# Kernel tuning notes

Measured on AMD Instinct MI355X. Metric: run time of the kernel, lower is better.

## Reference

```python
import jax, jax.numpy as jnp
import numpy as np
import math

B, C, H, W = 8, 64, 256, 256
E, NH = 256, 8
HD = E // NH  # 32


def get_coords(h, w):
    xx, yy = jnp.meshgrid(jnp.arange(h, dtype=jnp.float32), jnp.arange(w, dtype=jnp.float32), indexing='ij')
    return jnp.stack((xx.reshape(-1), yy.reshape(-1)), axis=-1)  # [N, 2]


def setup_inputs() -> dict:
    key = jax.random.key(0)
    ks = jax.random.split(key, 12)
    def xavier(k, shape):
        fan_out, fan_in = shape
        a = math.sqrt(6.0 / (fan_in + fan_out))
        return jax.random.uniform(k, shape, jnp.float32, -a, a)
    x = jax.random.normal(ks[0], (B, C, H, W), jnp.float32)
    z = jax.random.normal(ks[1], (B, C), jnp.float32)
    pos = jax.random.uniform(ks[2], (B, NH, 2), jnp.float32) * (H - 1)
    Wq = xavier(ks[3], (E, C)); bq = jnp.zeros((E,), jnp.float32)
    Wk = xavier(ks[4], (E, C)); bk = jnp.zeros((E,), jnp.float32)
    Wv = xavier(ks[5], (E, C)); bv = jnp.zeros((E,), jnp.float32)
    Wp = xavier(ks[6], (HD, 2)); bp = jax.random.uniform(ks[7], (HD,), jnp.float32, -1.0, 1.0) / math.sqrt(2.0)
    return {"x": x, "z": z, "pos": pos, "Wq": Wq, "bq": bq, "Wk": Wk, "bk": bk,
            "Wv": Wv, "bv": bv, "Wp": Wp, "bp": bp}


def reference(x, z, pos, Wq, bq, Wk, bk, Wv, bv, Wp, bp):
    b, c, h, w = x.shape
    n = h * w
    x_flat = x.reshape(b, c, n).transpose(0, 2, 1)          # [B, N, C]
    pos_grid = get_coords(h, w)                              # [N, 2]
    q = (z @ Wq.T + bq).reshape(b, NH, HD)                   # [B, H, hd]
    k = (x_flat @ Wk.T + bk).reshape(b, n, NH, HD)           # [B, N, H, hd]
    # relative-position modulation of keys
    rel = pos_grid[None, :, None, :] - pos[:, None, :, :]    # [B, N, H, 2]
    qxk = rel @ Wp.T + bp                                    # [B, N, H, hd]
    k = k * qxk
    v = x_flat @ Wv.T + bv                                   # [B, N, E]
    attn_logits = jnp.einsum('bhc,bnhc->bnh', q, k) / math.sqrt(HD)
    attention = jax.nn.softmax(attn_logits, axis=1)          # softmax over N
    pos_out = jnp.einsum('bnh,nx->bhx', attention, pos_grid) # [B, H, 2]
    values = jnp.einsum('bnh,bnc->bhc', attention, v)        # [B, H, E]
    return (values, pos_out)
```

## Files before the change

kernel.cpp:

```cpp
#include <hip/hip_runtime.h>

#define NN    65536
#define NSUB  256
#define NBLK  (NN/NSUB)
#define WPAD  260

#define OFF_W   0
#define SZ_W    (8*64*24)
#define OFF_CJ  (OFF_W + SZ_W)
#define SZ_CJ   (8*24)
#define OFF_PM  (OFF_CJ + SZ_CJ)
#define SZ_P    (8*NBLK*8)
#define OFF_PL  (OFF_PM + SZ_P)
#define OFF_PSP (OFF_PL + SZ_P)
#define OFF_PSX (OFF_PSP + 2*SZ_P)

#define SMEM1_FLOATS (64*WPAD + 8*256 + 1536 + 64)
#define SMEM1_BYTES  (SMEM1_FLOATS*4)

__global__ __launch_bounds__(64) void prep_kernel(
    const float* __restrict__ z,  const float* __restrict__ Wq, const float* __restrict__ bq,
    const float* __restrict__ Wk, const float* __restrict__ bk,
    const float* __restrict__ Wp, const float* __restrict__ bp,
    float* __restrict__ Weff, float* __restrict__ Cj)
{
  const int h = blockIdx.x, b = blockIdx.y, t = threadIdx.x;
  __shared__ float q[32];
  if (t < 32) {
    const int e = h*32 + t;
    float a = bq[e];
    const float* zr = z + b*64;
    const float* wr = Wq + e*64;
    #pragma unroll 8
    for (int c = 0; c < 64; ++c) a += zr[c]*wr[c];
    q[t] = a;
  }
  __syncthreads();
  {
    const int c = t;
    float w0 = 0.f, w1 = 0.f, w2 = 0.f;
    #pragma unroll 4
    for (int hd = 0; hd < 32; ++hd) {
      const float qk = q[hd] * Wk[(h*32+hd)*64 + c];
      w0 += qk * bp[hd];
      w1 += qk * Wp[hd*2+0];
      w2 += qk * Wp[hd*2+1];
    }
    float* o = Weff + (b*64 + c)*24 + h*3;
    o[0] = w0; o[1] = w1; o[2] = w2;
  }
  if (t < 3) {
    float s = 0.f;
    for (int hd = 0; hd < 32; ++hd) {
      const float m = (t == 0) ? bp[hd] : Wp[hd*2 + (t-1)];
      s += q[hd] * m * bk[h*32+hd];
    }
    Cj[b*24 + h*3 + t] = s;
  }
}

__global__ __launch_bounds__(256) void main_kernel(
    const float* __restrict__ x, const float* __restrict__ pos,
    const float* __restrict__ Weff, const float* __restrict__ Cj,
    float* __restrict__ Pm, float* __restrict__ Pl,
    float* __restrict__ Psp, float* __restrict__ Psx)
{
  extern __shared__ float sm[];
  float* xs  = sm;
  float* ps  = xs + 64*WPAD;
  float* wsw = ps + 8*256;
  float* red = wsw + 1536;
  const int t   = threadIdx.x;
  const int blk = blockIdx.x;
  const int b   = blockIdx.y;
  const int n0  = blk * NSUB;
  const int wid = t >> 6, lid = t & 63;

  {
    const float* xb = x + (size_t)b*64*NN + n0;
    #pragma unroll
    for (int r = 0; r < 16; ++r) {
      const int f  = t + r*256;
      const int c  = f >> 6;
      const int p4 = (f & 63) << 2;
      const float4 v = *(const float4*)(xb + (size_t)c*NN + p4);
      *(float4*)(xs + c*WPAD + p4) = v;
    }
    const float* wsrc = Weff + b*1536;
    #pragma unroll
    for (int r = 0; r < 6; ++r) wsw[t + r*256] = wsrc[t + r*256];
  }

  float cj[24];
  #pragma unroll
  for (int k = 0; k < 24; ++k) cj[k] = Cj[b*24 + k];
  float rxh[8], py[8];
  #pragma unroll
  for (int h = 0; h < 8; ++h) {
    rxh[h] = (float)blk - pos[(b*8+h)*2 + 0];
    py[h]  = pos[(b*8+h)*2 + 1];
  }

  __syncthreads();

  float2 acc2[12];
  #pragma unroll
  for (int j = 0; j < 12; ++j) acc2[j] = make_float2(cj[2*j], cj[2*j+1]);
  #pragma unroll 2
  for (int c = 0; c < 64; ++c) {
    const float xv = xs[c*WPAD + t];
    const float2* wr = (const float2*)(wsw + c*24);
    #pragma unroll
    for (int j = 0; j < 12; ++j) {
      acc2[j].x += wr[j].x * xv;
      acc2[j].y += wr[j].y * xv;
    }
  }
  const float* acc = (const float*)acc2;
  const float tyf = (float)t;
  float lg[8];
  #pragma unroll
  for (int h = 0; h < 8; ++h)
    lg[h] = (acc[h*3+0] + rxh[h]*acc[h*3+1] + (tyf - py[h])*acc[h*3+2]) * 0.17677669529663687f;

  float mh[8];
  #pragma unroll
  for (int h = 0; h < 8; ++h) {
    float m = lg[h];
    #pragma unroll
    for (int off = 32; off >= 1; off >>= 1) m = fmaxf(m, __shfl_xor(m, off, 64));
    mh[h] = m;
  }
  if (lid == 0) {
    #pragma unroll
    for (int h = 0; h < 8; ++h) red[h*4 + wid] = mh[h];
  }
  __syncthreads();

  #pragma unroll
  for (int h = 0; h < 8; ++h) {
    const float M = fmaxf(fmaxf(red[h*4+0], red[h*4+1]), fmaxf(red[h*4+2], red[h*4+3]));
    mh[h] = M;
    ps[h*256 + t] = __expf(lg[h] - M);
  }
  __syncthreads();

  {
    const int h0 = wid*2;
    const float4 pa = *(const float4*)(ps + h0*256 + 4*lid);
    const float4 pb = *(const float4*)(ps + (h0+1)*256 + 4*lid);
    const float j0 = (float)(4*lid);
    float s0a = pa.x + pa.y + pa.z + pa.w;
    float s1a = pa.x*j0 + pa.y*(j0+1.f) + pa.z*(j0+2.f) + pa.w*(j0+3.f);
    float s0b = pb.x + pb.y + pb.z + pb.w;
    float s1b = pb.x*j0 + pb.y*(j0+1.f) + pb.z*(j0+2.f) + pb.w*(j0+3.f);
    #pragma unroll
    for (int off = 32; off >= 1; off >>= 1) {
      s0a += __shfl_xor(s0a, off, 64);
      s1a += __shfl_xor(s1a, off, 64);
      s0b += __shfl_xor(s0b, off, 64);
      s1b += __shfl_xor(s1b, off, 64);
    }
    if (lid == 0) {
      const int base = (b*NBLK + blk)*8;
      const float blkf = (float)blk;
      Pm[base+h0]   = mh[h0];   Pl[base+h0]   = s0a;
      Psp[(base+h0)*2+0]   = blkf*s0a;  Psp[(base+h0)*2+1]   = s1a;
      Pm[base+h0+1] = mh[h0+1]; Pl[base+h0+1] = s0b;
      Psp[(base+h0+1)*2+0] = blkf*s0b;  Psp[(base+h0+1)*2+1] = s1b;
    }
  }

  float aB[8];
  #pragma unroll
  for (int h = 0; h < 8; ++h) aB[h] = 0.f;
  {
    const int nq = wid*64;
    const float* xr = xs + lid*WPAD + nq;
    #pragma unroll 2
    for (int j = 0; j < 16; ++j) {
      const float4 xv = *(const float4*)(xr + 4*j);
      #pragma unroll
      for (int h = 0; h < 8; ++h) {
        const float4 pv = *(const float4*)(ps + h*256 + nq + 4*j);
        aB[h] += pv.x*xv.x + pv.y*xv.y + pv.z*xv.z + pv.w*xv.w;
      }
    }
  }
  __syncthreads();
  {
    float* part = sm;
    #pragma unroll
    for (int h = 0; h < 8; ++h) part[(wid*8 + h)*64 + lid] = aB[h];
  }
  __syncthreads();
  {
    const int pb = (b*NBLK + blk)*8;
    #pragma unroll
    for (int r = 0; r < 2; ++r) {
      const int idx = t + 256*r;
      const float s = sm[idx] + sm[512+idx] + sm[1024+idx] + sm[1536+idx];
      Psx[(size_t)pb*64 + idx] = s;
    }
  }
}

__global__ __launch_bounds__(1024) void finish_kernel(
    const float* __restrict__ Pm, const float* __restrict__ Pl,
    const float* __restrict__ Psp, const float* __restrict__ Psx,
    const float* __restrict__ Wv, const float* __restrict__ bv,
    float* __restrict__ out)
{
  const int h = blockIdx.x, b = blockIdx.y, t = threadIdx.x;
  __shared__ float al[256];
  __shared__ float redm[32];
  __shared__ float sxl[1024];
  __shared__ float SXs[64];
  const int wid = t >> 6, lid = t & 63;

  float m_t = 0.f;
  if (t < 256) {
    m_t = Pm[(b*NBLK + t)*8 + h];
    float mm = m_t;
    #pragma unroll
    for (int off = 32; off >= 1; off >>= 1) mm = fmaxf(mm, __shfl_xor(mm, off, 64));
    if (lid == 0) redm[wid] = mm;
  }
  __syncthreads();
  const float M = fmaxf(fmaxf(redm[0], redm[1]), fmaxf(redm[2], redm[3]));
  if (t < 256) {
    const int pbase = (b*NBLK + t)*8 + h;
    const float a = __expf(m_t - M);
    al[t] = a;
    float lt  = Pl[pbase] * a;
    float sxt = Psp[pbase*2+0] * a;
    float syt = Psp[pbase*2+1] * a;
    #pragma unroll
    for (int off = 32; off >= 1; off >>= 1) {
      lt  += __shfl_xor(lt,  off, 64);
      sxt += __shfl_xor(sxt, off, 64);
      syt += __shfl_xor(syt, off, 64);
    }
    if (lid == 0) { redm[4+wid] = lt; redm[8+wid] = sxt; redm[12+wid] = syt; }
  }
  __syncthreads();
  const float L = redm[4]+redm[5]+redm[6]+redm[7];
  const float invL = 1.0f / L;

  {
    const int c = lid, g = wid;
    float acc = 0.f;
    #pragma unroll
    for (int k = 0; k < 16; ++k) {
      const int blk = g*16 + k;
      acc += Psx[((size_t)(b*NBLK + blk)*8 + h)*64 + c] * al[blk];
    }
    sxl[g*64 + c] = acc;
  }
  __syncthreads();
  if (t < 64) {
    float s = 0.f;
    #pragma unroll
    for (int g = 0; g < 16; ++g) s += sxl[g*64 + t];
    SXs[t] = s * invL;
  }
  __syncthreads();

  if (t < 256) {
    float v = bv[t];
    const float* wvr = Wv + t*64;
    #pragma unroll 8
    for (int c2 = 0; c2 < 64; ++c2) v += wvr[c2] * SXs[c2];
    out[(b*8+h)*256 + t] = v;
  }
  if (t == 0) {
    const float SPx = redm[8]+redm[9]+redm[10]+redm[11];
    const float SPy = redm[12]+redm[13]+redm[14]+redm[15];
    out[16384 + (b*8+h)*2 + 0] = SPx * invL;
    out[16384 + (b*8+h)*2 + 1] = SPy * invL;
  }
}

extern "C" void kernel_launch(void* const* d_in, const int* in_sizes, int n_in,
                              void* d_out, int out_size, void* d_ws, size_t ws_size,
                              hipStream_t stream)
{
  const float* x   = (const float*)d_in[0];
  const float* z   = (const float*)d_in[1];
  const float* pos = (const float*)d_in[2];
  const float* Wq  = (const float*)d_in[3];
  const float* bq  = (const float*)d_in[4];
  const float* Wk  = (const float*)d_in[5];
  const float* bk  = (const float*)d_in[6];
  const float* Wv  = (const float*)d_in[7];
  const float* bv  = (const float*)d_in[8];
  const float* Wp  = (const float*)d_in[9];
  const float* bp  = (const float*)d_in[10];
  float* out = (float*)d_out;
  float* ws  = (float*)d_ws;

  float* Weff = ws + OFF_W;
  float* Cj   = ws + OFF_CJ;
  float* Pm   = ws + OFF_PM;
  float* Pl   = ws + OFF_PL;
  float* Psp  = ws + OFF_PSP;
  float* Psx  = ws + OFF_PSX;

  (void)hipFuncSetAttribute((const void*)main_kernel,
                            hipFuncAttributeMaxDynamicSharedMemorySize, SMEM1_BYTES);

  prep_kernel  <<<dim3(8,8),    64,   0,           stream>>>(z, Wq, bq, Wk, bk, Wp, bp, Weff, Cj);
  main_kernel  <<<dim3(NBLK,8), 256,  SMEM1_BYTES, stream>>>(x, pos, Weff, Cj, Pm, Pl, Psp, Psx);
  finish_kernel<<<dim3(8,8),    1024, 0,           stream>>>(Pm, Pl, Psp, Psx, Wv, bv, out);
}
```

Baseline: 264.7 us.

## Load x into registers, use wave readlane for P·x, split final reduction

The main kernel now has each thread load its own 64 channel values straight into registers and compute the logits from those, reading the weight rows directly from global memory. x is stored transposed in shared memory with odd padding. The P·x product broadcasts softmax weights across the wave with readlane instead of staging them in shared memory, and the per-block sums are built from wave shuffles. The single 64-block finish kernel becomes a two-stage reduction across 512 blocks and then 64 blocks, to spread the merge of partials over more of the GPU. The trade-offs are higher register pressure from the 64-float array, uncached-style weight reads from global, and one extra kernel launch.

```diff
diff --git a/kernel.cpp b/kernel.cpp
--- a/kernel.cpp
+++ b/kernel.cpp
@@ -3,7 +3,7 @@
 #define NN    65536
 #define NSUB  256
 #define NBLK  (NN/NSUB)
-#define WPAD  260
+#define CPAD  65
 
 #define OFF_W   0
 #define SZ_W    (8*64*24)
@@ -14,8 +14,11 @@
 #define OFF_PL  (OFF_PM + SZ_P)
 #define OFF_PSP (OFF_PL + SZ_P)
 #define OFF_PSX (OFF_PSP + 2*SZ_P)
-
-#define SMEM1_FLOATS (64*WPAD + 8*256 + 1536 + 64)
+#define SZ_PSX  (8*NBLK*8*64)
+#define OFF_Q   (OFF_PSX + SZ_PSX)
+#define QSTR    68
+
+#define SMEM1_FLOATS (NSUB*CPAD + 128)
 #define SMEM1_BYTES  (SMEM1_FLOATS*4)
 
 __global__ __launch_bounds__(64) void prep_kernel(
@@ -59,7 +62,7 @@
   }
 }
 
-__global__ __launch_bounds__(256) void main_kernel(
+__global__ __launch_bounds__(256, 2) void main_kernel(
     const float* __restrict__ x, const float* __restrict__ pos,
     const float* __restrict__ Weff, const float* __restrict__ Cj,
     float* __restrict__ Pm, float* __restrict__ Pl,
@@ -67,132 +70,115 @@
 {
   extern __shared__ float sm[];
   float* xs  = sm;
-  float* ps  = xs + 64*WPAD;
-  float* wsw = ps + 8*256;
-  float* red = wsw + 1536;
+  float* red = sm + NSUB*CPAD;
   const int t   = threadIdx.x;
   const int blk = blockIdx.x;
   const int b   = blockIdx.y;
   const int n0  = blk * NSUB;
   const int wid = t >> 6, lid = t & 63;
 
-  {
-    const float* xb = x + (size_t)b*64*NN + n0;
-    #pragma unroll
-    for (int r = 0; r < 16; ++r) {
-      const int f  = t + r*256;
-      const int c  = f >> 6;
-      const int p4 = (f & 63) << 2;
-      const float4 v = *(const float4*)(xb + (size_t)c*NN + p4);
-      *(float4*)(xs + c*WPAD + p4) = v;
-    }
-    const float* wsrc = Weff + b*1536;
-    #pragma unroll
-    for (int r = 0; r < 6; ++r) wsw[t + r*256] = wsrc[t + r*256];
-  }
-
-  float cj[24];
-  #pragma unroll
-  for (int k = 0; k < 24; ++k) cj[k] = Cj[b*24 + k];
-  float rxh[8], py[8];
-  #pragma unroll
-  for (int h = 0; h < 8; ++h) {
-    rxh[h] = (float)blk - pos[(b*8+h)*2 + 0];
-    py[h]  = pos[(b*8+h)*2 + 1];
-  }
-
-  __syncthreads();
-
-  float2 acc2[12];
-  #pragma unroll
-  for (int j = 0; j < 12; ++j) acc2[j] = make_float2(cj[2*j], cj[2*j+1]);
-  #pragma unroll 2
-  for (int c = 0; c < 64; ++c) {
-    const float xv = xs[c*WPAD + t];
-    const float2* wr = (const float2*)(wsw + c*24);
-    #pragma unroll
-    for (int j = 0; j < 12; ++j) {
-      acc2[j].x += wr[j].x * xv;
-      acc2[j].y += wr[j].y * xv;
-    }
-  }
-  const float* acc = (const float*)acc2;
-  const float tyf = (float)t;
+  float vx[64];
+  {
+    const float* xg = x + (size_t)b*64*NN + n0 + t;
+    #pragma unroll
+    for (int c = 0; c < 64; ++c) vx[c] = xg[(size_t)c*NN];
+    #pragma unroll
+    for (int c = 0; c < 64; ++c) xs[t*CPAD + c] = vx[c];
+  }
+
+  float acc[24];
+  {
+    const float* cjp = Cj + b*24;
+    #pragma unroll
+    for (int k = 0; k < 24; ++k) acc[k] = cjp[k];
+  }
+  {
+    const float* wb = Weff + b*1536;
+    #pragma unroll
+    for (int c = 0; c < 64; ++c) {
+      const float xv = vx[c];
+      const float* wr = wb + c*24;
+      #pragma unroll
+      for (int k = 0; k < 24; ++k) acc[k] += wr[k]*xv;
+    }
+  }
   float lg[8];
-  #pragma unroll
-  for (int h = 0; h < 8; ++h)
-    lg[h] = (acc[h*3+0] + rxh[h]*acc[h*3+1] + (tyf - py[h])*acc[h*3+2]) * 0.17677669529663687f;
-
-  float mh[8];
+  {
+    const float gx = (float)blk;
+    const float ty = (float)t;
+    #pragma unroll
+    for (int h = 0; h < 8; ++h) {
+      const float rx = gx - pos[(b*8+h)*2 + 0];
+      const float ry = ty - pos[(b*8+h)*2 + 1];
+      lg[h] = (acc[h*3+0] + rx*acc[h*3+1] + ry*acc[h*3+2]) * 0.17677669529663687f;
+    }
+  }
+
   #pragma unroll
   for (int h = 0; h < 8; ++h) {
     float m = lg[h];
     #pragma unroll
     for (int off = 32; off >= 1; off >>= 1) m = fmaxf(m, __shfl_xor(m, off, 64));
-    mh[h] = m;
-  }
-  if (lid == 0) {
-    #pragma unroll
-    for (int h = 0; h < 8; ++h) red[h*4 + wid] = mh[h];
-  }
-  __syncthreads();
-
+    if (lid == 0) red[h*4 + wid] = m;
+  }
+  __syncthreads();
+
+  float p[8];
   #pragma unroll
   for (int h = 0; h < 8; ++h) {
     const float M = fmaxf(fmaxf(red[h*4+0], red[h*4+1]), fmaxf(red[h*4+2], red[h*4+3]));
-    mh[h] = M;
-    ps[h*256 + t] = __expf(lg[h] - M);
-  }
-  __syncthreads();
-
-  {
-    const int h0 = wid*2;
-    const float4 pa = *(const float4*)(ps + h0*256 + 4*lid);
-    const float4 pb = *(const float4*)(ps + (h0+1)*256 + 4*lid);
-    const float j0 = (float)(4*lid);
-    float s0a = pa.x + pa.y + pa.z + pa.w;
-    float s1a = pa.x*j0 + pa.y*(j0+1.f) + pa.z*(j0+2.f) + pa.w*(j0+3.f);
-    float s0b = pb.x + pb.y + pb.z + pb.w;
-    float s1b = pb.x*j0 + pb.y*(j0+1.f) + pb.z*(j0+2.f) + pb.w*(j0+3.f);
-    #pragma unroll
-    for (int off = 32; off >= 1; off >>= 1) {
-      s0a += __shfl_xor(s0a, off, 64);
-      s1a += __shfl_xor(s1a, off, 64);
-      s0b += __shfl_xor(s0b, off, 64);
-      s1b += __shfl_xor(s1b, off, 64);
-    }
-    if (lid == 0) {
-      const int base = (b*NBLK + blk)*8;
-      const float blkf = (float)blk;
-      Pm[base+h0]   = mh[h0];   Pl[base+h0]   = s0a;
-      Psp[(base+h0)*2+0]   = blkf*s0a;  Psp[(base+h0)*2+1]   = s1a;
-      Pm[base+h0+1] = mh[h0+1]; Pl[base+h0+1] = s0b;
-      Psp[(base+h0+1)*2+0] = blkf*s0b;  Psp[(base+h0+1)*2+1] = s1b;
-    }
+    p[h] = __expf(lg[h] - M);
+  }
+  {
+    const float lf = (float)lid;
+    #pragma unroll
+    for (int h = 0; h < 8; ++h) {
+      float sp  = p[h];
+      float spj = p[h]*lf;
+      #pragma unroll
+      for (int off = 32; off >= 1; off >>= 1) {
+        sp  += __shfl_xor(sp,  off, 64);
+        spj += __shfl_xor(spj, off, 64);
+      }
+      if (lid == 0) { red[32 + h*4 + wid] = sp; red[64 + h*4 + wid] = spj; }
+    }
+  }
+  __syncthreads();
+
+  if (t < 8) {
+    const int base = (b*NBLK + blk)*8 + t;
+    const float M = fmaxf(fmaxf(red[t*4+0], red[t*4+1]), fmaxf(red[t*4+2], red[t*4+3]));
+    float L = 0.f, SJ = 0.f;
+    #pragma unroll
+    for (int w = 0; w < 4; ++w) {
+      const float sp = red[32 + t*4 + w];
+      L  += sp;
+      SJ += 64.0f*(float)w*sp + red[64 + t*4 + w];
+    }
+    Pm[base] = M;
+    Pl[base] = L;
+    Psp[base*2+0] = (float)blk * L;
+    Psp[base*2+1] = SJ;
   }
 
   float aB[8];
   #pragma unroll
   for (int h = 0; h < 8; ++h) aB[h] = 0.f;
   {
-    const int nq = wid*64;
-    const float* xr = xs + lid*WPAD + nq;
-    #pragma unroll 2
-    for (int j = 0; j < 16; ++j) {
-      const float4 xv = *(const float4*)(xr + 4*j);
+    const float* xcol = xs + wid*64*CPAD + lid;
+    #pragma unroll 8
+    for (int j = 0; j < 64; ++j) {
+      const float xv = xcol[j*CPAD];
       #pragma unroll
       for (int h = 0; h < 8; ++h) {
-        const float4 pv = *(const float4*)(ps + h*256 + nq + 4*j);
-        aB[h] += pv.x*xv.x + pv.y*xv.y + pv.z*xv.z + pv.w*xv.w;
+        const float pj = __int_as_float(__builtin_amdgcn_readlane(__float_as_int(p[h]), j));
+        aB[h] = fmaf(pj, xv, aB[h]);
       }
     }
   }
   __syncthreads();
-  {
-    float* part = sm;
-    #pragma unroll
-    for (int h = 0; h < 8; ++h) part[(wid*8 + h)*64 + lid] = aB[h];
-  }
+  #pragma unroll
+  for (int h = 0; h < 8; ++h) sm[(wid*8 + h)*64 + lid] = aB[h];
   __syncthreads();
   {
     const int pb = (b*NBLK + blk)*8;
@@ -205,79 +191,108 @@
   }
 }
 
-__global__ __launch_bounds__(1024) void finish_kernel(
+__global__ __launch_bounds__(256) void reduce1_kernel(
     const float* __restrict__ Pm, const float* __restrict__ Pl,
     const float* __restrict__ Psp, const float* __restrict__ Psx,
-    const float* __restrict__ Wv, const float* __restrict__ bv,
+    float* __restrict__ Q)
+{
+  const int g = blockIdx.x, h = blockIdx.y, b = blockIdx.z, t = threadIdx.x;
+  __shared__ float al[32];
+  __shared__ float mgs;
+  __shared__ float sums[3];
+  __shared__ float sxl[256];
+  const int base = (b*NBLK + g*32)*8 + h;
+
+  float m_t = -1e30f;
+  if (t < 32) m_t = Pm[base + t*8];
+  if (t < 64) {
+    float mm = m_t;
+    #pragma unroll
+    for (int off = 16; off >= 1; off >>= 1) mm = fmaxf(mm, __shfl_xor(mm, off, 64));
+    if (t == 0) mgs = mm;
+  }
+  __syncthreads();
+  const float Mg = mgs;
+  if (t < 32) {
+    const float a = __expf(m_t - Mg);
+    al[t] = a;
+    float lt  = Pl[base + t*8] * a;
+    float sx  = Psp[(base + t*8)*2 + 0] * a;
+    float sy  = Psp[(base + t*8)*2 + 1] * a;
+    #pragma unroll
+    for (int off = 16; off >= 1; off >>= 1) {
+      lt += __shfl_xor(lt, off, 64);
+      sx += __shfl_xor(sx, off, 64);
+      sy += __shfl_xor(sy, off, 64);
+    }
+    if (t == 0) { sums[0] = lt; sums[1] = sx; sums[2] = sy; }
+  }
+  __syncthreads();
+  {
+    const int c = t & 63, g2 = t >> 6;
+    float acc = 0.f;
+    #pragma unroll
+    for (int i = 0; i < 8; ++i) {
+      const int k = g2*8 + i;
+      acc += al[k] * Psx[(size_t)(base + k*8)*64 + c];
+    }
+    sxl[g2*64 + c] = acc;
+  }
+  __syncthreads();
+  float* q = Q + ((b*8 + h)*8 + g)*QSTR;
+  if (t < 64) q[4+t] = sxl[t] + sxl[64+t] + sxl[128+t] + sxl[192+t];
+  if (t == 0) { q[0] = Mg; q[1] = sums[0]; q[2] = sums[1]; q[3] = sums[2]; }
+}
+
+__global__ __launch_bounds__(64) void reduce2_kernel(
+    const float* __restrict__ Q, const float* __restrict__ Wv, const float* __restrict__ bv,
     float* __restrict__ out)
 {
   const int h = blockIdx.x, b = blockIdx.y, t = threadIdx.x;
-  __shared__ float al[256];
-  __shared__ float redm[32];
-  __shared__ float sxl[1024];
+  __shared__ float qm[8], bl[8], l8[8], sx8[8], sy8[8];
   __shared__ float SXs[64];
-  const int wid = t >> 6, lid = t & 63;
-
-  float m_t = 0.f;
-  if (t < 256) {
-    m_t = Pm[(b*NBLK + t)*8 + h];
-    float mm = m_t;
-    #pragma unroll
-    for (int off = 32; off >= 1; off >>= 1) mm = fmaxf(mm, __shfl_xor(mm, off, 64));
-    if (lid == 0) redm[wid] = mm;
-  }
-  __syncthreads();
-  const float M = fmaxf(fmaxf(redm[0], redm[1]), fmaxf(redm[2], redm[3]));
-  if (t < 256) {
-    const int pbase = (b*NBLK + t)*8 + h;
-    const float a = __expf(m_t - M);
-    al[t] = a;
-    float lt  = Pl[pbase] * a;
-    float sxt = Psp[pbase*2+0] * a;
-    float syt = Psp[pbase*2+1] * a;
-    #pragma unroll
-    for (int off = 32; off >= 1; off >>= 1) {
-      lt  += __shfl_xor(lt,  off, 64);
-      sxt += __shfl_xor(sxt, off, 64);
-      syt += __shfl_xor(syt, off, 64);
-    }
-    if (lid == 0) { redm[4+wid] = lt; redm[8+wid] = sxt; redm[12+wid] = syt; }
-  }
-  __syncthreads();
-  const float L = redm[4]+redm[5]+redm[6]+redm[7];
+  const float* qb = Q + ((b*8 + h)*8)*QSTR;
+
+  if (t < 8) qm[t] = qb[t*QSTR + 0];
+  __syncthreads();
+  float M = qm[0];
+  #pragma unroll
+  for (int g = 1; g < 8; ++g) M = fmaxf(M, qm[g]);
+  if (t < 8) {
+    const float be = __expf(qm[t] - M);
+    bl[t]  = be;
+    l8[t]  = be * qb[t*QSTR + 1];
+    sx8[t] = be * qb[t*QSTR + 2];
+    sy8[t] = be * qb[t*QSTR + 3];
+  }
+  __syncthreads();
+  float L = 0.f;
+  #pragma unroll
+  for (int g = 0; g < 8; ++g) L += l8[g];
   const float invL = 1.0f / L;
-
-  {
-    const int c = lid, g = wid;
-    float acc = 0.f;
-    #pragma unroll
-    for (int k = 0; k < 16; ++k) {
-      const int blk = g*16 + k;
-      acc += Psx[((size_t)(b*NBLK + blk)*8 + h)*64 + c] * al[blk];
-    }
-    sxl[g*64 + c] = acc;
-  }
-  __syncthreads();
-  if (t < 64) {
+  {
     float s = 0.f;
     #pragma unroll
-    for (int g = 0; g < 16; ++g) s += sxl[g*64 + t];
+    for (int g = 0; g < 8; ++g) s += bl[g] * qb[g*QSTR + 4 + t];
     SXs[t] = s * invL;
   }
   __syncthreads();
 
-  if (t < 256) {
-    float v = bv[t];
-    const float* wvr = Wv + t*64;
+  #pragma unroll
+  for (int r = 0; r < 4; ++r) {
+    const int e = t + 64*r;
+    float v = bv[e];
+    const float* wvr = Wv + e*64;
     #pragma unroll 8
-    for (int c2 = 0; c2 < 64; ++c2) v += wvr[c2] * SXs[c2];
-    out[(b*8+h)*256 + t] = v;
+    for (int c = 0; c < 64; ++c) v += wvr[c] * SXs[c];
+    out[(b*8 + h)*256 + e] = v;
   }
   if (t == 0) {
-    const float SPx = redm[8]+redm[9]+redm[10]+redm[11];
-    const float SPy = redm[12]+redm[13]+redm[14]+redm[15];
-    out[16384 + (b*8+h)*2 + 0] = SPx * invL;
-    out[16384 + (b*8+h)*2 + 1] = SPy * invL;
+    float spx = 0.f, spy = 0.f;
+    #pragma unroll
+    for (int g = 0; g < 8; ++g) { spx += sx8[g]; spy += sy8[g]; }
+    out[16384 + (b*8 + h)*2 + 0] = spx * invL;
+    out[16384 + (b*8 + h)*2 + 1] = spy * invL;
   }
 }
 
@@ -305,11 +320,13 @@
   float* Pl   = ws + OFF_PL;
   float* Psp  = ws + OFF_PSP;
   float* Psx  = ws + OFF_PSX;
+  float* Q    = ws + OFF_Q;
 
   (void)hipFuncSetAttribute((const void*)main_kernel,
                             hipFuncAttributeMaxDynamicSharedMemorySize, SMEM1_BYTES);
 
-  prep_kernel  <<<dim3(8,8),    64,   0,           stream>>>(z, Wq, bq, Wk, bk, Wp, bp, Weff, Cj);
-  main_kernel  <<<dim3(NBLK,8), 256,  SMEM1_BYTES, stream>>>(x, pos, Weff, Cj, Pm, Pl, Psp, Psx);
-  finish_kernel<<<dim3(8,8),    1024, 0,           stream>>>(Pm, Pl, Psp, Psx, Wv, bv, out);
-}
+  prep_kernel   <<<dim3(8,8),     64,  0,           stream>>>(z, Wq, bq, Wk, bk, Wp, bp, Weff, Cj);
+  main_kernel   <<<dim3(NBLK,8),  256, SMEM1_BYTES, stream>>>(x, pos, Weff, Cj, Pm, Pl, Psp, Psx);
+  reduce1_kernel<<<dim3(8,8,8),   256, 0,           stream>>>(Pm, Pl, Psp, Psx, Q);
+  reduce2_kernel<<<dim3(8,8),     64,  0,           stream>>>(Q, Wv, bv, out);
+}
```

New measurement: 506.8 us. 91.4% more time.
